# Kernel optimization log

Measured on AMD Instinct MI355X. Metric: run time of the kernel, lower is better.

The kernel has to match this reference:

```python
import jax, jax.numpy as jnp
import numpy as np

EPS = 1e-5
N_HEADS = 8
NEG = -1e32


def _pos_emb(S, D):
    # CosinePositionalEmbedding: sin/cos fully overwrite the random init for even D
    pos = jnp.arange(S, dtype=jnp.float32)[:, None]
    div = jnp.exp(jnp.arange(0, D, 2, dtype=jnp.float32) * (-np.log(10000.0) / D))
    pe = jnp.zeros((S, D), dtype=jnp.float32)
    pe = pe.at[:, 0::2].set(jnp.sin(pos * div))
    pe = pe.at[:, 1::2].set(jnp.cos(pos * div))
    return pe


def _ln(x, g, b):
    mu = jnp.mean(x, axis=-1, keepdims=True)
    var = jnp.mean((x - mu) ** 2, axis=-1, keepdims=True)
    return (x - mu) / jnp.sqrt(var + EPS) * g + b


def setup_inputs() -> dict:
    key = jax.random.key(0)
    B, S, D, FF, L = 32, 512, 512, 2048, 4
    ks = jax.random.split(key, 8)
    w = 0.02
    return {
        "q_embed_data": jax.random.normal(ks[0], (B, S, D), jnp.float32),
        "qa_embed_data": jax.random.normal(ks[1], (B, S, D), jnp.float32),
        "boost_focus": jax.random.uniform(ks[2], (1,), jnp.float32),
        "Wk": w * jax.random.normal(ks[3], (L, D, D), jnp.float32),
        "bk": jnp.zeros((L, D), jnp.float32),
        "Wv": w * jax.random.normal(ks[4], (L, D, D), jnp.float32),
        "bv": jnp.zeros((L, D), jnp.float32),
        "Wo": w * jax.random.normal(ks[5], (L, D, D), jnp.float32),
        "bo": jnp.zeros((L, D), jnp.float32),
        "ln1_g": jnp.ones((L, D), jnp.float32),
        "ln1_b": jnp.zeros((L, D), jnp.float32),
        "W1": w * jax.random.normal(ks[6], (L, D, FF), jnp.float32),
        "b1": jnp.zeros((L, FF), jnp.float32),
        "W2": w * jax.random.normal(ks[7], (L, FF, D), jnp.float32),
        "b2": jnp.zeros((L, D), jnp.float32),
        "ln2_g": jnp.ones((L, D), jnp.float32),
        "ln2_b": jnp.zeros((L, D), jnp.float32),
    }


def reference(q_embed_data, qa_embed_data, boost_focus, Wk, bk, Wv, bv, Wo, bo,
              ln1_g, ln1_b, W1, b1, W2, b2, ln2_g, ln2_b):
    B, S, D = q_embed_data.shape
    L = Wk.shape[0]
    H = N_HEADS
    dk = D // H
    bf = boost_focus[0]
    pe = _pos_emb(S, D)
    x = q_embed_data + pe[None]          # query/key stream
    y = qa_embed_data + pe[None]         # value stream (fixed across blocks)
    # mask=0: triu(k=0)==0 -> only strictly past positions (j < i) allowed
    allowed = jnp.tril(jnp.ones((S, S), bool), k=-1)
    scale = 1.0 / np.sqrt(dk)
    for l in range(L):
        # kq_same=True: q and k both use k_linear on x -> identical projections
        qk = (x @ Wk[l] + bk[l]).reshape(B, S, H, dk).transpose(0, 2, 1, 3)
        v = (y @ Wv[l] + bv[l]).reshape(B, S, H, dk).transpose(0, 2, 1, 3)
        scores = jnp.einsum('bhid,bhjd->bhij', qk, qk) * scale * (1.0 + bf)
        scores = jnp.where(allowed, scores, NEG)
        probs = jax.nn.softmax(scores, axis=-1)
        probs = probs.at[:, :, 0, :].set(0.0)  # zero_pad: first query row zeroed
        attn = jnp.einsum('bhij,bhjd->bhid', probs, v)
        attn = attn.transpose(0, 2, 1, 3).reshape(B, S, D) @ Wo[l] + bo[l]
        x = _ln(x + attn, ln1_g[l], ln1_b[l])
        ff = jax.nn.relu(x @ W1[l] + b1[l]) @ W2[l] + b2[l]
        x = _ln(x + ff, ln2_g[l], ln2_b[l])
    return x
```

## Files before the change

### kernel.cpp

```cpp
#include <hip/hip_runtime.h>
#include <hip/hip_bf16.h>

typedef __bf16 bf16_t;
typedef __bf16 bf16x4 __attribute__((ext_vector_type(4)));
typedef __bf16 bf16x8 __attribute__((ext_vector_type(8)));
typedef float f32x4 __attribute__((ext_vector_type(4)));

union FragU { bf16x8 v; bf16x4 h[2]; };
union F4U { float4 v; float f[4]; };

constexpr int BB = 32, SS = 512, DD = 512, FFD = 2048, LL = 4, HH = 8;

__device__ __forceinline__ int permk(int k) {
  int g = (k >> 2) & 7;
  int pos = (g < 4) ? (g << 1) : (((g - 4) << 1) | 1);
  return (k & ~31) | (pos << 2) | (k & 3);
}

__device__ __forceinline__ void gload_lds16(const bf16_t* g, bf16_t* l) {
  __builtin_amdgcn_global_load_lds(
      (const __attribute__((address_space(1))) void*)g,
      (__attribute__((address_space(3))) void*)l, 16, 0, 0);
}

template<int N> __device__ __forceinline__ void vmwait() {
  asm volatile("s_waitcnt vmcnt(%0)" :: "n"(N) : "memory");
}
__device__ __forceinline__ void lgkmwait0() {
  asm volatile("s_waitcnt lgkmcnt(0)" ::: "memory");
}
__device__ __forceinline__ void barrier_raw() {
  asm volatile("s_barrier" ::: "memory");
}

#define MFMA_ACC(d, a, b) d = __builtin_amdgcn_mfma_f32_16x16x32_bf16((a).v, (b).v, d, 0, 0, 0)

__global__ void pe_kernel(float* __restrict__ pe) {
  int idx = blockIdx.x * blockDim.x + threadIdx.x;
  if (idx >= SS * DD / 2) return;
  int p = idx % (DD / 2);
  int s = idx / (DD / 2);
  float div = expf((float)(2 * p) * (-9.210340371976184f / (float)DD));
  float a = (float)s * div;
  pe[s * DD + 2 * p]     = sinf(a);
  pe[s * DD + 2 * p + 1] = cosf(a);
}

__global__ __launch_bounds__(256) void tcast_kernel(const float* __restrict__ src,
                                                    bf16_t* __restrict__ dst,
                                                    int K, int N) {
  __shared__ float tile[32][33];
  size_t mat = (size_t)blockIdx.z * (size_t)K * (size_t)N;
  int k0 = blockIdx.y * 32, n0 = blockIdx.x * 32;
  int t = threadIdx.x;
  int r = t >> 3, c4 = (t & 7) * 4;
  const float4 v = *reinterpret_cast<const float4*>(&src[mat + (size_t)(k0 + r) * N + n0 + c4]);
  tile[r][c4 + 0] = v.x; tile[r][c4 + 1] = v.y; tile[r][c4 + 2] = v.z; tile[r][c4 + 3] = v.w;
  __syncthreads();
  bf16x4 o;
  o[0] = (bf16_t)tile[c4 + 0][r];
  o[1] = (bf16_t)tile[c4 + 1][r];
  o[2] = (bf16_t)tile[c4 + 2][r];
  o[3] = (bf16_t)tile[c4 + 3][r];
  *reinterpret_cast<bf16x4*>(&dst[mat + permk((n0 + r) * K + k0 + c4)]) = o;
}

__global__ void addpe_kernel(const float* __restrict__ q, const float* __restrict__ qa,
                             const float* __restrict__ pe,
                             float* __restrict__ x, bf16_t* __restrict__ xb,
                             bf16_t* __restrict__ yb) {
  int i = blockIdx.x * blockDim.x + threadIdx.x;
  int pei = i & (SS * DD / 4 - 1);
  float4 pv = reinterpret_cast<const float4*>(pe)[pei];
  float4 qv = reinterpret_cast<const float4*>(q)[i];
  float4 av = reinterpret_cast<const float4*>(qa)[i];
  float4 xv = make_float4(qv.x + pv.x, qv.y + pv.y, qv.z + pv.z, qv.w + pv.w);
  float4 yv = make_float4(av.x + pv.x, av.y + pv.y, av.z + pv.z, av.w + pv.w);
  reinterpret_cast<float4*>(x)[i] = xv;
  bf16x4 xo, yo;
  xo[0] = (bf16_t)xv.x; xo[1] = (bf16_t)xv.y; xo[2] = (bf16_t)xv.z; xo[3] = (bf16_t)xv.w;
  yo[0] = (bf16_t)yv.x; yo[1] = (bf16_t)yv.y; yo[2] = (bf16_t)yv.z; yo[3] = (bf16_t)yv.w;
  int kp = permk(4 * i);
  *reinterpret_cast<bf16x4*>(&xb[kp]) = xo;
  *reinterpret_cast<bf16x4*>(&yb[kp]) = yo;
}

template<int OMODE, bool RELU>
__global__ __launch_bounds__(256, 2) void gemm_kernel(const bf16_t* __restrict__ A,
                                                      const bf16_t* __restrict__ Bt,
                                                      const float* __restrict__ bias,
                                                      void* __restrict__ Cout,
                                                      int N, int K, int nnt) {
  __shared__ bf16_t a_s[2][128 * 64];
  __shared__ bf16_t b_s[2][128 * 64];
  const int t = threadIdx.x;
  const int nwg = gridDim.x;
  const int bid = blockIdx.x;
  const int wg = (bid & 7) * (nwg >> 3) + (bid >> 3);
  const int m0 = (wg / nnt) * 128, n0 = (wg % nnt) * 128;
  const int l = t & 63, w = t >> 6, g = l >> 4, ln = l & 15;
  const int wm = (w >> 1) * 64, wn = (w & 1) * 64;
  const int tr = t >> 3;
  const int bsrc = ((t & 7) ^ (tr & 7)) * 8;
  const bf16_t* Asrc = A + (size_t)(m0 + tr) * K + bsrc;
  const bf16_t* Bsrc = Bt + (size_t)(n0 + tr) * K + bsrc;
  const size_t rstr = (size_t)32 * K;
  const int x0 = (g ^ (ln & 7)) * 8;
  const int x1 = ((4 + g) ^ (ln & 7)) * 8;

  auto STAGE = [&](int p, int T) {
    const int k0 = T << 6;
#pragma unroll
    for (int i = 0; i < 4; i++) gload_lds16(Asrc + k0 + i * rstr, &a_s[p][(i * 256 + t) * 8]);
#pragma unroll
    for (int i = 0; i < 4; i++) gload_lds16(Bsrc + k0 + i * rstr, &b_s[p][(i * 256 + t) * 8]);
  };

  f32x4 acc[4][4] = {};
  const int NT = K >> 6;
  STAGE(0, 0);
  STAGE(1, 1);
  for (int T = 0; T < NT; T++) {
    const int p = T & 1;
    if (T + 1 < NT) vmwait<8>(); else vmwait<0>();
    barrier_raw();
    __builtin_amdgcn_sched_barrier(0);
#pragma unroll
    for (int kc = 0; kc < 2; kc++) {
      const int xo = kc ? x1 : x0;
      FragU fa[4], fb[4];
#pragma unroll
      for (int mi = 0; mi < 4; mi++)
        fa[mi].v = *reinterpret_cast<const bf16x8*>(&a_s[p][(wm + mi * 16 + ln) * 64 + xo]);
#pragma unroll
      for (int ni = 0; ni < 4; ni++)
        fb[ni].v = *reinterpret_cast<const bf16x8*>(&b_s[p][(wn + ni * 16 + ln) * 64 + xo]);
      __builtin_amdgcn_s_setprio(1);
#pragma unroll
      for (int mi = 0; mi < 4; mi++)
#pragma unroll
        for (int ni = 0; ni < 4; ni++)
          MFMA_ACC(acc[mi][ni], fa[mi], fb[ni]);
      __builtin_amdgcn_s_setprio(0);
    }
    __builtin_amdgcn_sched_barrier(0);
    barrier_raw();
    if (T + 2 < NT) STAGE(p, T + 2);
  }

  if constexpr (OMODE == 2) {
    const int brow = m0 >> 9;
    const int s0b = (m0 & 511) + wm;
    bf16_t* vout = reinterpret_cast<bf16_t*>(Cout);
#pragma unroll
    for (int ni = 0; ni < 4; ni++) {
      const int d = n0 + wn + ni * 16 + ln;
      const float bv = bias[d];
      const int h = d >> 6, dd = d & 63;
      bf16_t* vrow = vout + ((size_t)((brow * HH + h) * 64 + dd)) * SS;
#pragma unroll
      for (int mi = 0; mi < 4; mi++) {
        const int s0 = s0b + mi * 16 + g * 4;
        const int jt = s0 >> 6, jj = s0 & 63;
        const int js = jj >> 5, half = (jj >> 4) & 1;
        const int blkx = (js * 4 + g) ^ (dd & 7);
        bf16x4 o;
#pragma unroll
        for (int r = 0; r < 4; r++) o[r] = (bf16_t)(acc[mi][ni][r] + bv);
        *reinterpret_cast<bf16x4*>(&vrow[jt * 64 + blkx * 8 + half * 4]) = o;
      }
    }
  } else {
#pragma unroll
    for (int ni = 0; ni < 4; ni++) {
      const int col = n0 + wn + ni * 16 + ln;
      const float bv = bias[col];
      const int colp = (OMODE == 1) ? permk(col) : col;
#pragma unroll
      for (int mi = 0; mi < 4; mi++)
#pragma unroll
        for (int r = 0; r < 4; r++) {
          int row = m0 + wm + mi * 16 + g * 4 + r;
          float o = acc[mi][ni][r] + bv;
          if (RELU) o = fmaxf(o, 0.f);
          if (OMODE == 1)
            reinterpret_cast<bf16_t*>(Cout)[(size_t)row * N + colp] = (bf16_t)o;
          else
            reinterpret_cast<float*>(Cout)[(size_t)row * N + col] = o;
        }
    }
  }
}

__global__ __launch_bounds__(512, 1) void gemmW_kernel(const bf16_t* __restrict__ A,
                                                       const bf16_t* __restrict__ Bt,
                                                       const float* __restrict__ bias,
                                                       bf16_t* __restrict__ Cout,
                                                       int N, int K, int nnt) {
  __shared__ bf16_t a_s[2][256 * 64];
  __shared__ bf16_t b_s[2][256 * 64];
  const int t = threadIdx.x;
  const int bid = blockIdx.x, nwg = gridDim.x;
  const int wg = (bid & 7) * (nwg >> 3) + (bid >> 3);
  const int m0 = (wg / nnt) * 256, n0 = (wg % nnt) * 256;
  const int l = t & 63, w = t >> 6, g = l >> 4, ln = l & 15, lnx = l & 7;
  const int wr = w >> 2, wc = w & 3;
  const int tr = t >> 3;
  const int bsrc = ((t & 7) ^ (tr & 7)) * 8;
  const bf16_t* Asrc = A + (size_t)(m0 + tr) * K + bsrc;
  const bf16_t* Bsrc = Bt + (size_t)(n0 + tr) * K + bsrc;
  const size_t rstr = (size_t)64 * K;
  const int x0 = (g ^ lnx) * 8;
  const int x1 = ((4 + g) ^ lnx) * 8;

  auto STA = [&](int q, int T2, int i) {
    gload_lds16(Asrc + (T2 << 6) + i * rstr, &a_s[q][(i * 512 + t) * 8]);
  };
  auto STB = [&](int q, int T2, int i) {
    gload_lds16(Bsrc + (T2 << 6) + i * rstr, &b_s[q][(i * 512 + t) * 8]);
  };

  f32x4 acc[8][4] = {};
  const int NT = K >> 6;
#pragma unroll
  for (int i = 0; i < 4; i++) { STA(0, 0, i); STB(0, 0, i); }
#pragma unroll
  for (int i = 0; i < 4; i++) { STA(1, 1, i); STB(1, 1, i); }
  vmwait<8>();
  barrier_raw();

  for (int T = 0; T < NT; T++) {
    const int p = T & 1;
    const bool st = (T + 2) < NT;
    FragU fa[4], fb[4];
#pragma unroll
    for (int mf = 0; mf < 4; mf++)
      fa[mf].v = *reinterpret_cast<const bf16x8*>(&a_s[p][(wr * 128 + mf * 16 + ln) * 64 + x0]);
#pragma unroll
    for (int nf = 0; nf < 4; nf++)
      fb[nf].v = *reinterpret_cast<const bf16x8*>(&b_s[p][(wc * 64 + nf * 16 + ln) * 64 + x0]);
    barrier_raw();
    lgkmwait0();
    __builtin_amdgcn_sched_barrier(0);
    __builtin_amdgcn_s_setprio(1);
#pragma unroll
    for (int mf = 0; mf < 4; mf++)
#pragma unroll
      for (int nf = 0; nf < 4; nf++) MFMA_ACC(acc[mf][nf], fa[mf], fb[nf]);
    __builtin_amdgcn_s_setprio(0);
    barrier_raw();
#pragma unroll
    for (int mf = 0; mf < 4; mf++)
      fa[mf].v = *reinterpret_cast<const bf16x8*>(&a_s[p][(wr * 128 + 64 + mf * 16 + ln) * 64 + x0]);
    barrier_raw();
    lgkmwait0();
    __builtin_amdgcn_sched_barrier(0);
    __builtin_amdgcn_s_setprio(1);
#pragma unroll
    for (int mf = 0; mf < 4; mf++)
#pragma unroll
      for (int nf = 0; nf < 4; nf++) MFMA_ACC(acc[4 + mf][nf], fa[mf], fb[nf]);
    __builtin_amdgcn_s_setprio(0);
    barrier_raw();
#pragma unroll
    for (int mf = 0; mf < 4; mf++)
      fa[mf].v = *reinterpret_cast<const bf16x8*>(&a_s[p][(wr * 128 + mf * 16 + ln) * 64 + x1]);
#pragma unroll
    for (int nf = 0; nf < 4; nf++)
      fb[nf].v = *reinterpret_cast<const bf16x8*>(&b_s[p][(wc * 64 + nf * 16 + ln) * 64 + x1]);
    barrier_raw();
    if (st) { STA(p, T + 2, 0); STA(p, T + 2, 2); STB(p, T + 2, 0); STB(p, T + 2, 1); STB(p, T + 2, 2); STB(p, T + 2, 3); }
    lgkmwait0();
    __builtin_amdgcn_sched_barrier(0);
    __builtin_amdgcn_s_setprio(1);
#pragma unroll
    for (int mf = 0; mf < 4; mf++)
#pragma unroll
      for (int nf = 0; nf < 4; nf++) MFMA_ACC(acc[mf][nf], fa[mf], fb[nf]);
    __builtin_amdgcn_s_setprio(0);
    barrier_raw();
#pragma unroll
    for (int mf = 0; mf < 4; mf++)
      fa[mf].v = *reinterpret_cast<const bf16x8*>(&a_s[p][(wr * 128 + 64 + mf * 16 + ln) * 64 + x1]);
    barrier_raw();
    if (st) { STA(p, T + 2, 1); STA(p, T + 2, 3); }
    lgkmwait0();
    __builtin_amdgcn_sched_barrier(0);
    __builtin_amdgcn_s_setprio(1);
#pragma unroll
    for (int mf = 0; mf < 4; mf++)
#pragma unroll
      for (int nf = 0; nf < 4; nf++) MFMA_ACC(acc[4 + mf][nf], fa[mf], fb[nf]);
    __builtin_amdgcn_s_setprio(0);
    if (T + 1 < NT) { if (st) vmwait<8>(); else vmwait<0>(); }
    barrier_raw();
  }

#pragma unroll
  for (int nf = 0; nf < 4; nf++) {
    const int col = n0 + wc * 64 + nf * 16 + ln;
    const float bv = bias[col];
    const int colp = permk(col);
#pragma unroll
    for (int mf = 0; mf < 8; mf++)
#pragma unroll
      for (int r = 0; r < 4; r++) {
        int row = m0 + wr * 128 + mf * 16 + g * 4 + r;
        float o = fmaxf(acc[mf][nf][r] + bv, 0.f);
        Cout[(size_t)row * N + colp] = (bf16_t)o;
      }
  }
}

__global__ __launch_bounds__(256) void ln_kernel(const float* __restrict__ xin,
                                                 const float* __restrict__ addv,
                                                 const float* __restrict__ gamma,
                                                 const float* __restrict__ beta,
                                                 float* __restrict__ xout,
                                                 bf16_t* __restrict__ xbout) {
  int row = blockIdx.x * 4 + (threadIdx.x >> 6);
  int l = threadIdx.x & 63;
  const float* px = xin + (size_t)row * DD;
  const float* pa = addv + (size_t)row * DD;
  float vals[8];
  float s = 0.f;
#pragma unroll
  for (int i = 0; i < 2; i++) {
    float4 a = reinterpret_cast<const float4*>(px)[l * 2 + i];
    float4 b = reinterpret_cast<const float4*>(pa)[l * 2 + i];
    vals[i * 4 + 0] = a.x + b.x;
    vals[i * 4 + 1] = a.y + b.y;
    vals[i * 4 + 2] = a.z + b.z;
    vals[i * 4 + 3] = a.w + b.w;
  }
#pragma unroll
  for (int j = 0; j < 8; j++) s += vals[j];
#pragma unroll
  for (int off = 1; off < 64; off <<= 1) s += __shfl_xor(s, off, 64);
  float mean = s * (1.f / DD);
  float sq = 0.f;
#pragma unroll
  for (int j = 0; j < 8; j++) { float d = vals[j] - mean; sq += d * d; }
#pragma unroll
  for (int off = 1; off < 64; off <<= 1) sq += __shfl_xor(sq, off, 64);
  float rstd = rsqrtf(sq * (1.f / DD) + 1e-5f);
#pragma unroll
  for (int i = 0; i < 2; i++) {
    F4U o; bf16x4 ob;
#pragma unroll
    for (int j = 0; j < 4; j++) {
      int colj = l * 8 + i * 4 + j;
      float v = (vals[i * 4 + j] - mean) * rstd * gamma[colj] + beta[colj];
      o.f[j] = v;
      ob[j] = (bf16_t)v;
    }
    reinterpret_cast<float4*>(xout + (size_t)row * DD)[l * 2 + i] = o.v;
    *reinterpret_cast<bf16x4*>(&xbout[(size_t)row * DD + permk(l * 8 + i * 4)]) = ob;
  }
}

__global__ __launch_bounds__(256) void attn_kernel(const bf16_t* __restrict__ qk,
                                                   const bf16_t* __restrict__ vtg,
                                                   bf16_t* __restrict__ outp,
                                                   const float* __restrict__ bfp) {
  __shared__ bf16_t k_s[2][64 * 64];
  __shared__ bf16_t v_t[2][64 * 64];
  const int bx = blockIdx.x, h = blockIdx.y, b = blockIdx.z;
  const int t = threadIdx.x, l = t & 63, w = t >> 6, g = l >> 4, ln = l & 15;
  const float sc = 0.125f * (1.f + bfp[0]);
  const size_t base = ((size_t)b * SS) * DD + h * 64;
  const bf16_t* vbase = vtg + ((size_t)((b * HH + h) * 64)) * SS;
  const int NQT = SS / 64;

  auto STAGEKV = [&](int q, int j0) {
    int c1 = t + 256;
    int jr0 = t >> 3, bb0 = t & 7;
    int jr1 = c1 >> 3, bb1 = c1 & 7;
    gload_lds16(qk + base + (size_t)(j0 + jr0) * DD + ((bb0 ^ (jr0 & 7)) * 8), &k_s[q][t * 8]);
    gload_lds16(qk + base + (size_t)(j0 + jr1) * DD + ((bb1 ^ (jr1 & 7)) * 8), &k_s[q][c1 * 8]);
    gload_lds16(vbase + (size_t)jr0 * SS + j0 + bb0 * 8, &v_t[q][t * 8]);
    gload_lds16(vbase + (size_t)jr1 * SS + j0 + bb1 * 8, &v_t[q][c1 * 8]);
  };

  for (int pass = 0; pass < 2; pass++) {
    const int qt = pass ? (NQT - 1 - bx) : bx;
    const int i0 = qt * 64;
    STAGEKV(0, 0);
    FragU qB[2];
    {
      const bf16_t* qp = qk + base + (size_t)(i0 + w * 16 + ln) * DD;
      qB[0].v = *reinterpret_cast<const bf16x8*>(&qp[g * 8]);
      qB[1].v = *reinterpret_cast<const bf16x8*>(&qp[32 + g * 8]);
    }
    float m = -1e30f, lrow = 0.f;
    f32x4 acc[4] = {};
    const int iql = w * 16 + ln;

    for (int kt = 0; kt <= qt; kt++) {
      const int j0 = kt * 64;
      const int p = kt & 1;
      if (kt < qt) { STAGEKV(p ^ 1, j0 + 64); vmwait<4>(); }
      else vmwait<0>();
      barrier_raw();
      __builtin_amdgcn_sched_barrier(0);
      f32x4 sfr[4] = {};
#pragma unroll
      for (int ks = 0; ks < 2; ks++)
#pragma unroll
        for (int nj = 0; nj < 4; nj++) {
          int jc = nj * 16 + ln;
          FragU ka;
          ka.v = *reinterpret_cast<const bf16x8*>(&k_s[p][jc * 64 + (((ks * 4 + g) ^ (jc & 7)) * 8)]);
          sfr[nj] = __builtin_amdgcn_mfma_f32_16x16x32_bf16(ka.v, qB[ks].v, sfr[nj], 0, 0, 0);
        }
      if (kt == qt) {
#pragma unroll
        for (int nj = 0; nj < 4; nj++)
#pragma unroll
          for (int r = 0; r < 4; r++)
            if (nj * 16 + g * 4 + r >= iql) sfr[nj][r] = -1e30f;
      }
      float pm = -1e30f;
#pragma unroll
      for (int nj = 0; nj < 4; nj++)
#pragma unroll
        for (int r = 0; r < 4; r++) pm = fmaxf(pm, sfr[nj][r]);
      pm = fmaxf(pm, __shfl_xor(pm, 16, 64));
      pm = fmaxf(pm, __shfl_xor(pm, 32, 64));
      float mnew = fmaxf(m, pm);
      float fac = __expf(sc * (m - mnew));
      m = mnew;
      float ps = 0.f;
#pragma unroll
      for (int nj = 0; nj < 4; nj++)
#pragma unroll
        for (int r = 0; r < 4; r++) {
          float p2 = __expf(sc * (sfr[nj][r] - m));
          sfr[nj][r] = p2;
          ps += p2;
        }
      ps += __shfl_xor(ps, 16, 64);
      ps += __shfl_xor(ps, 32, 64);
      lrow = lrow * fac + ps;
      float facr[4];
#pragma unroll
      for (int r = 0; r < 4; r++) facr[r] = __shfl(fac, g * 4 + r, 64);
#pragma unroll
      for (int nd = 0; nd < 4; nd++)
#pragma unroll
        for (int r = 0; r < 4; r++) acc[nd][r] *= facr[r];
      FragU pa[2];
#pragma unroll
      for (int js = 0; js < 2; js++)
#pragma unroll
        for (int kk = 0; kk < 4; kk++) {
          pa[js].v[kk]     = (bf16_t)sfr[js * 2][kk];
          pa[js].v[kk + 4] = (bf16_t)sfr[js * 2 + 1][kk];
        }
#pragma unroll
      for (int js = 0; js < 2; js++)
#pragma unroll
        for (int nd = 0; nd < 4; nd++) {
          int d = nd * 16 + ln;
          FragU vb;
          vb.v = *reinterpret_cast<const bf16x8*>(&v_t[p][d * 64 + (((js * 4 + g) ^ (d & 7)) * 8)]);
          acc[nd] = __builtin_amdgcn_mfma_f32_16x16x32_bf16(pa[js].v, vb.v, acc[nd], 0, 0, 0);
        }
      barrier_raw();
    }
    float lr[4];
#pragma unroll
    for (int r = 0; r < 4; r++) lr[r] = __shfl(lrow, g * 4 + r, 64);
    const int orow0 = i0 + w * 16 + g * 4;
#pragma unroll
    for (int nd = 0; nd < 4; nd++) {
      const int colp = permk(nd * 16 + ln);
#pragma unroll
      for (int r = 0; r < 4; r++) {
        int grow = orow0 + r;
        float o = (grow > 0 && lr[r] > 0.f) ? acc[nd][r] / lr[r] : 0.f;
        outp[base + (size_t)grow * DD + colp] = (bf16_t)o;
      }
    }
  }
}

extern "C" void kernel_launch(void* const* d_in, const int* in_sizes, int n_in,
                              void* d_out, int out_size, void* d_ws, size_t ws_size,
                              hipStream_t stream) {
  const float* q_emb  = (const float*)d_in[0];
  const float* qa_emb = (const float*)d_in[1];
  const float* bfp    = (const float*)d_in[2];
  const float* Wk  = (const float*)d_in[3];
  const float* bk  = (const float*)d_in[4];
  const float* Wv  = (const float*)d_in[5];
  const float* bv  = (const float*)d_in[6];
  const float* Wo  = (const float*)d_in[7];
  const float* bo  = (const float*)d_in[8];
  const float* g1  = (const float*)d_in[9];
  const float* be1 = (const float*)d_in[10];
  const float* W1  = (const float*)d_in[11];
  const float* b1  = (const float*)d_in[12];
  const float* W2  = (const float*)d_in[13];
  const float* b2  = (const float*)d_in[14];
  const float* g2  = (const float*)d_in[15];
  const float* be2 = (const float*)d_in[16];
  float* out = (float*)d_out;
  (void)in_sizes; (void)n_in; (void)out_size; (void)ws_size;

  char* wsp = (char*)d_ws;
  size_t off = 0;
  auto alloc = [&](size_t bytes) -> void* {
    void* p = wsp + off;
    off += (bytes + 255) & ~(size_t)255;
    return p;
  };
  const size_t BSD = (size_t)BB * SS * DD;
  float*  pe   = (float*) alloc((size_t)SS * DD * 4);
  float*  x    = (float*) alloc(BSD * 4);
  float*  tmp  = (float*) alloc(BSD * 4);
  bf16_t* xb   = (bf16_t*)alloc(BSD * 2);
  bf16_t* yb   = (bf16_t*)alloc(BSD * 2);
  bf16_t* qkb  = (bf16_t*)alloc(BSD * 2);
  bf16_t* vtg  = (bf16_t*)alloc(BSD * 2);
  bf16_t* atb  = (bf16_t*)alloc(BSD * 2);
  bf16_t* h1   = (bf16_t*)alloc((size_t)BB * SS * FFD * 2);
  bf16_t* Wkb  = (bf16_t*)alloc((size_t)LL * DD * DD * 2);
  bf16_t* Wvb  = (bf16_t*)alloc((size_t)LL * DD * DD * 2);
  bf16_t* Wob  = (bf16_t*)alloc((size_t)LL * DD * DD * 2);
  bf16_t* W1b  = (bf16_t*)alloc((size_t)LL * DD * FFD * 2);
  bf16_t* W2b  = (bf16_t*)alloc((size_t)LL * FFD * DD * 2);

  pe_kernel<<<(SS * DD / 2 + 255) / 256, 256, 0, stream>>>(pe);
  tcast_kernel<<<dim3(DD / 32, DD / 32, LL), 256, 0, stream>>>(Wk, Wkb, DD, DD);
  tcast_kernel<<<dim3(DD / 32, DD / 32, LL), 256, 0, stream>>>(Wv, Wvb, DD, DD);
  tcast_kernel<<<dim3(DD / 32, DD / 32, LL), 256, 0, stream>>>(Wo, Wob, DD, DD);
  tcast_kernel<<<dim3(FFD / 32, DD / 32, LL), 256, 0, stream>>>(W1, W1b, DD, FFD);
  tcast_kernel<<<dim3(DD / 32, FFD / 32, LL), 256, 0, stream>>>(W2, W2b, FFD, DD);
  addpe_kernel<<<(int)(BSD / 4 / 256), 256, 0, stream>>>(q_emb, qa_emb, pe, x, xb, yb);

  const int M = BB * SS;
  const int nD = (M / 128) * (DD / 128);
  const int nW = (M / 256) * (FFD / 256);
  dim3 gA(SS / 128, HH, BB);
  for (int layer = 0; layer < LL; layer++) {
    const bf16_t* Wkl = Wkb + (size_t)layer * DD * DD;
    const bf16_t* Wvl = Wvb + (size_t)layer * DD * DD;
    const bf16_t* Wol = Wob + (size_t)layer * DD * DD;
    const bf16_t* W1l = W1b + (size_t)layer * DD * FFD;
    const bf16_t* W2l = W2b + (size_t)layer * FFD * DD;
    gemm_kernel<1, false><<<nD, 256, 0, stream>>>(xb, Wkl, bk + layer * DD, qkb, DD, DD, DD / 128);
    gemm_kernel<2, false><<<nD, 256, 0, stream>>>(yb, Wvl, bv + layer * DD, vtg, DD, DD, DD / 128);
    attn_kernel<<<gA, 256, 0, stream>>>(qkb, vtg, atb, bfp);
    gemm_kernel<0, false><<<nD, 256, 0, stream>>>(atb, Wol, bo + layer * DD, tmp, DD, DD, DD / 128);
    ln_kernel<<<M / 4, 256, 0, stream>>>(x, tmp, g1 + layer * DD, be1 + layer * DD, x, xb);
    gemmW_kernel<<<nW, 512, 0, stream>>>(xb, W1l, b1 + layer * FFD, h1, FFD, DD, FFD / 256);
    gemm_kernel<0, false><<<nD, 256, 0, stream>>>(h1, W2l, b2 + layer * DD, tmp, DD, FFD, DD / 128);
    float* xo = (layer == LL - 1) ? out : x;
    ln_kernel<<<M / 4, 256, 0, stream>>>(x, tmp, g2 + layer * DD, be2 + layer * DD, xo, xb);
  }
}
```

Measured before the change: 887.3 us.

## Keep residual stream in bf16, tile FFN hidden layout, permute LN params

Drops the fp32 residual copy x and the fp32 tmp buffer. LayerNorm now reads bf16 residual and bf16 GEMM output in the permuted column layout, using gamma/beta that are pre-permuted once to match. The W1 GEMM writes h1 in 256x256 tiles that the W2 GEMM reads through a new tiled A-addressing mode, aiming for contiguous loads. This cuts memory traffic in the LN and GEMM epilogues, but the residual now accumulates in bf16, which can cost accuracy.

```diff
diff --git a/kernel.cpp b/kernel.cpp
--- a/kernel.cpp
+++ b/kernel.cpp
@@ -15,6 +15,11 @@
   int g = (k >> 2) & 7;
   int pos = (g < 4) ? (g << 1) : (((g - 4) << 1) | 1);
   return (k & ~31) | (pos << 2) | (k & 3);
+}
+__device__ __forceinline__ int permpos(int c) {
+  int gq = c >> 2;
+  int pos = (gq < 4) ? (gq << 1) : (((gq - 4) << 1) | 1);
+  return pos * 4 + (c & 3);
 }
 
 __device__ __forceinline__ void gload_lds16(const bf16_t* g, bf16_t* l) {
@@ -44,6 +49,16 @@
   float a = (float)s * div;
   pe[s * DD + 2 * p]     = sinf(a);
   pe[s * DD + 2 * p + 1] = cosf(a);
+}
+
+__global__ void gbperm_kernel(const float* __restrict__ g1, const float* __restrict__ b1,
+                              const float* __restrict__ g2, const float* __restrict__ b2,
+                              float* __restrict__ g1p, float* __restrict__ b1p,
+                              float* __restrict__ g2p, float* __restrict__ b2p) {
+  int idx = blockIdx.x * 256 + threadIdx.x;
+  if (idx >= LL * DD) return;
+  int p = (idx & ~511) | permk(idx & 511);
+  g1p[p] = g1[idx]; b1p[p] = b1[idx]; g2p[p] = g2[idx]; b2p[p] = b2[idx];
 }
 
 __global__ __launch_bounds__(256) void tcast_kernel(const float* __restrict__ src,
@@ -67,25 +82,23 @@
 
 __global__ void addpe_kernel(const float* __restrict__ q, const float* __restrict__ qa,
                              const float* __restrict__ pe,
-                             float* __restrict__ x, bf16_t* __restrict__ xb,
-                             bf16_t* __restrict__ yb) {
+                             bf16_t* __restrict__ xb, bf16_t* __restrict__ yb) {
   int i = blockIdx.x * blockDim.x + threadIdx.x;
   int pei = i & (SS * DD / 4 - 1);
   float4 pv = reinterpret_cast<const float4*>(pe)[pei];
   float4 qv = reinterpret_cast<const float4*>(q)[i];
   float4 av = reinterpret_cast<const float4*>(qa)[i];
-  float4 xv = make_float4(qv.x + pv.x, qv.y + pv.y, qv.z + pv.z, qv.w + pv.w);
-  float4 yv = make_float4(av.x + pv.x, av.y + pv.y, av.z + pv.z, av.w + pv.w);
-  reinterpret_cast<float4*>(x)[i] = xv;
   bf16x4 xo, yo;
-  xo[0] = (bf16_t)xv.x; xo[1] = (bf16_t)xv.y; xo[2] = (bf16_t)xv.z; xo[3] = (bf16_t)xv.w;
-  yo[0] = (bf16_t)yv.x; yo[1] = (bf16_t)yv.y; yo[2] = (bf16_t)yv.z; yo[3] = (bf16_t)yv.w;
+  xo[0] = (bf16_t)(qv.x + pv.x); xo[1] = (bf16_t)(qv.y + pv.y);
+  xo[2] = (bf16_t)(qv.z + pv.z); xo[3] = (bf16_t)(qv.w + pv.w);
+  yo[0] = (bf16_t)(av.x + pv.x); yo[1] = (bf16_t)(av.y + pv.y);
+  yo[2] = (bf16_t)(av.z + pv.z); yo[3] = (bf16_t)(av.w + pv.w);
   int kp = permk(4 * i);
   *reinterpret_cast<bf16x4*>(&xb[kp]) = xo;
   *reinterpret_cast<bf16x4*>(&yb[kp]) = yo;
 }
 
-template<int OMODE, bool RELU>
+template<int OMODE, bool RELU, bool ATILED = false>
 __global__ __launch_bounds__(256, 2) void gemm_kernel(const bf16_t* __restrict__ A,
                                                       const bf16_t* __restrict__ Bt,
                                                       const float* __restrict__ bias,
@@ -102,18 +115,27 @@
   const int wm = (w >> 1) * 64, wn = (w & 1) * 64;
   const int tr = t >> 3;
   const int bsrc = ((t & 7) ^ (tr & 7)) * 8;
-  const bf16_t* Asrc = A + (size_t)(m0 + tr) * K + bsrc;
+  const bf16_t* Asrc;
+  size_t arstr;
+  if constexpr (ATILED) {
+    Asrc = A + (size_t)(m0 >> 8) * ((size_t)K * 256) + (size_t)((m0 & 255) + tr) * 256 + bsrc;
+    arstr = 8192;
+  } else {
+    Asrc = A + (size_t)(m0 + tr) * K + bsrc;
+    arstr = (size_t)32 * K;
+  }
   const bf16_t* Bsrc = Bt + (size_t)(n0 + tr) * K + bsrc;
   const size_t rstr = (size_t)32 * K;
   const int x0 = (g ^ (ln & 7)) * 8;
   const int x1 = ((4 + g) ^ (ln & 7)) * 8;
 
   auto STAGE = [&](int p, int T) {
-    const int k0 = T << 6;
-#pragma unroll
-    for (int i = 0; i < 4; i++) gload_lds16(Asrc + k0 + i * rstr, &a_s[p][(i * 256 + t) * 8]);
-#pragma unroll
-    for (int i = 0; i < 4; i++) gload_lds16(Bsrc + k0 + i * rstr, &b_s[p][(i * 256 + t) * 8]);
+    const int ka = ATILED ? ((T >> 2) * 65536 + (T & 3) * 64) : (T << 6);
+    const int kb = T << 6;
+#pragma unroll
+    for (int i = 0; i < 4; i++) gload_lds16(Asrc + ka + i * arstr, &a_s[p][(i * 256 + t) * 8]);
+#pragma unroll
+    for (int i = 0; i < 4; i++) gload_lds16(Bsrc + kb + i * rstr, &b_s[p][(i * 256 + t) * 8]);
   };
 
   f32x4 acc[4][4] = {};
@@ -175,7 +197,7 @@
     for (int ni = 0; ni < 4; ni++) {
       const int col = n0 + wn + ni * 16 + ln;
       const float bv = bias[col];
-      const int colp = (OMODE == 1) ? permk(col) : col;
+      const int colp = permk(col);
 #pragma unroll
       for (int mi = 0; mi < 4; mi++)
 #pragma unroll
@@ -183,10 +205,7 @@
           int row = m0 + wm + mi * 16 + g * 4 + r;
           float o = acc[mi][ni][r] + bv;
           if (RELU) o = fmaxf(o, 0.f);
-          if (OMODE == 1)
-            reinterpret_cast<bf16_t*>(Cout)[(size_t)row * N + colp] = (bf16_t)o;
-          else
-            reinterpret_cast<float*>(Cout)[(size_t)row * N + col] = o;
+          reinterpret_cast<bf16_t*>(Cout)[(size_t)row * N + colp] = (bf16_t)o;
         }
     }
   }
@@ -296,45 +315,41 @@
     barrier_raw();
   }
 
+  const size_t tbase = (size_t)(m0 >> 8) * ((size_t)N * 256) + (size_t)(n0 >> 8) * 65536;
 #pragma unroll
   for (int nf = 0; nf < 4; nf++) {
-    const int col = n0 + wc * 64 + nf * 16 + ln;
-    const float bv = bias[col];
-    const int colp = permk(col);
-#pragma unroll
-    for (int mf = 0; mf < 8; mf++)
+    const int col_l = wc * 64 + nf * 16 + ln;
+    const float bv = bias[n0 + col_l];
+    const int colp = (col_l & ~31) | permpos(col_l & 31);
+#pragma unroll
+    for (int mf = 0; mf < 8; mf++) {
+      const int mloc = wr * 128 + mf * 16 + g * 4;
 #pragma unroll
       for (int r = 0; r < 4; r++) {
-        int row = m0 + wr * 128 + mf * 16 + g * 4 + r;
         float o = fmaxf(acc[mf][nf][r] + bv, 0.f);
-        Cout[(size_t)row * N + colp] = (bf16_t)o;
+        Cout[tbase + (size_t)(mloc + r) * 256 + colp] = (bf16_t)o;
       }
-  }
-}
-
-__global__ __launch_bounds__(256) void ln_kernel(const float* __restrict__ xin,
-                                                 const float* __restrict__ addv,
-                                                 const float* __restrict__ gamma,
-                                                 const float* __restrict__ beta,
-                                                 float* __restrict__ xout,
-                                                 bf16_t* __restrict__ xbout) {
+    }
+  }
+}
+
+template<bool FINAL>
+__global__ __launch_bounds__(256) void lnp_kernel(const bf16_t* __restrict__ xb,
+                                                  const bf16_t* __restrict__ tb,
+                                                  const float* __restrict__ gp,
+                                                  const float* __restrict__ bp,
+                                                  bf16_t* __restrict__ xbo,
+                                                  float* __restrict__ fout) {
   int row = blockIdx.x * 4 + (threadIdx.x >> 6);
   int l = threadIdx.x & 63;
-  const float* px = xin + (size_t)row * DD;
-  const float* pa = addv + (size_t)row * DD;
+  size_t base = (size_t)row * DD + l * 8;
+  FragU xv, tv;
+  xv.v = *reinterpret_cast<const bf16x8*>(&xb[base]);
+  tv.v = *reinterpret_cast<const bf16x8*>(&tb[base]);
   float vals[8];
   float s = 0.f;
 #pragma unroll
-  for (int i = 0; i < 2; i++) {
-    float4 a = reinterpret_cast<const float4*>(px)[l * 2 + i];
-    float4 b = reinterpret_cast<const float4*>(pa)[l * 2 + i];
-    vals[i * 4 + 0] = a.x + b.x;
-    vals[i * 4 + 1] = a.y + b.y;
-    vals[i * 4 + 2] = a.z + b.z;
-    vals[i * 4 + 3] = a.w + b.w;
-  }
-#pragma unroll
-  for (int j = 0; j < 8; j++) s += vals[j];
+  for (int j = 0; j < 8; j++) { vals[j] = (float)xv.v[j] + (float)tv.v[j]; s += vals[j]; }
 #pragma unroll
   for (int off = 1; off < 64; off <<= 1) s += __shfl_xor(s, off, 64);
   float mean = s * (1.f / DD);
@@ -344,18 +359,29 @@
 #pragma unroll
   for (int off = 1; off < 64; off <<= 1) sq += __shfl_xor(sq, off, 64);
   float rstd = rsqrtf(sq * (1.f / DD) + 1e-5f);
-#pragma unroll
-  for (int i = 0; i < 2; i++) {
-    F4U o; bf16x4 ob;
-#pragma unroll
-    for (int j = 0; j < 4; j++) {
-      int colj = l * 8 + i * 4 + j;
-      float v = (vals[i * 4 + j] - mean) * rstd * gamma[colj] + beta[colj];
-      o.f[j] = v;
-      ob[j] = (bf16_t)v;
-    }
-    reinterpret_cast<float4*>(xout + (size_t)row * DD)[l * 2 + i] = o.v;
-    *reinterpret_cast<bf16x4*>(&xbout[(size_t)row * DD + permk(l * 8 + i * 4)]) = ob;
+  F4U g0, g1q, b0, b1q;
+  g0.v  = *reinterpret_cast<const float4*>(&gp[l * 8]);
+  g1q.v = *reinterpret_cast<const float4*>(&gp[l * 8 + 4]);
+  b0.v  = *reinterpret_cast<const float4*>(&bp[l * 8]);
+  b1q.v = *reinterpret_cast<const float4*>(&bp[l * 8 + 4]);
+  float ov[8];
+#pragma unroll
+  for (int j = 0; j < 4; j++) ov[j]     = (vals[j] - mean) * rstd * g0.f[j] + b0.f[j];
+#pragma unroll
+  for (int j = 0; j < 4; j++) ov[4 + j] = (vals[4 + j] - mean) * rstd * g1q.f[j] + b1q.f[j];
+  if (FINAL) {
+    int c = l >> 2, i = l & 3;
+    F4U o0, o1;
+#pragma unroll
+    for (int j = 0; j < 4; j++) { o0.f[j] = ov[j]; o1.f[j] = ov[4 + j]; }
+    float* fr = fout + (size_t)row * DD + c * 32 + 4 * i;
+    *reinterpret_cast<float4*>(fr) = o0.v;
+    *reinterpret_cast<float4*>(fr + 16) = o1.v;
+  } else {
+    FragU ob;
+#pragma unroll
+    for (int j = 0; j < 8; j++) ob.v[j] = (bf16_t)ov[j];
+    *reinterpret_cast<bf16x8*>(&xbo[base]) = ob.v;
   }
 }
 
@@ -517,14 +543,17 @@
   };
   const size_t BSD = (size_t)BB * SS * DD;
   float*  pe   = (float*) alloc((size_t)SS * DD * 4);
-  float*  x    = (float*) alloc(BSD * 4);
-  float*  tmp  = (float*) alloc(BSD * 4);
   bf16_t* xb   = (bf16_t*)alloc(BSD * 2);
   bf16_t* yb   = (bf16_t*)alloc(BSD * 2);
   bf16_t* qkb  = (bf16_t*)alloc(BSD * 2);
   bf16_t* vtg  = (bf16_t*)alloc(BSD * 2);
   bf16_t* atb  = (bf16_t*)alloc(BSD * 2);
+  bf16_t* tmpb = (bf16_t*)alloc(BSD * 2);
   bf16_t* h1   = (bf16_t*)alloc((size_t)BB * SS * FFD * 2);
+  float*  g1p  = (float*) alloc((size_t)LL * DD * 4);
+  float*  b1p  = (float*) alloc((size_t)LL * DD * 4);
+  float*  g2p  = (float*) alloc((size_t)LL * DD * 4);
+  float*  b2p  = (float*) alloc((size_t)LL * DD * 4);
   bf16_t* Wkb  = (bf16_t*)alloc((size_t)LL * DD * DD * 2);
   bf16_t* Wvb  = (bf16_t*)alloc((size_t)LL * DD * DD * 2);
   bf16_t* Wob  = (bf16_t*)alloc((size_t)LL * DD * DD * 2);
@@ -532,12 +561,13 @@
   bf16_t* W2b  = (bf16_t*)alloc((size_t)LL * FFD * DD * 2);
 
   pe_kernel<<<(SS * DD / 2 + 255) / 256, 256, 0, stream>>>(pe);
+  gbperm_kernel<<<(LL * DD + 255) / 256, 256, 0, stream>>>(g1, be1, g2, be2, g1p, b1p, g2p, b2p);
   tcast_kernel<<<dim3(DD / 32, DD / 32, LL), 256, 0, stream>>>(Wk, Wkb, DD, DD);
   tcast_kernel<<<dim3(DD / 32, DD / 32, LL), 256, 0, stream>>>(Wv, Wvb, DD, DD);
   tcast_kernel<<<dim3(DD / 32, DD / 32, LL), 256, 0, stream>>>(Wo, Wob, DD, DD);
   tcast_kernel<<<dim3(FFD / 32, DD / 32, LL), 256, 0, stream>>>(W1, W1b, DD, FFD);
   tcast_kernel<<<dim3(DD / 32, FFD / 32, LL), 256, 0, stream>>>(W2, W2b, FFD, DD);
-  addpe_kernel<<<(int)(BSD / 4 / 256), 256, 0, stream>>>(q_emb, qa_emb, pe, x, xb, yb);
+  addpe_kernel<<<(int)(BSD / 4 / 256), 256, 0, stream>>>(q_emb, qa_emb, pe, xb, yb);
 
   const int M = BB * SS;
   const int nD = (M / 128) * (DD / 128);
@@ -552,11 +582,13 @@
     gemm_kernel<1, false><<<nD, 256, 0, stream>>>(xb, Wkl, bk + layer * DD, qkb, DD, DD, DD / 128);
     gemm_kernel<2, false><<<nD, 256, 0, stream>>>(yb, Wvl, bv + layer * DD, vtg, DD, DD, DD / 128);
     attn_kernel<<<gA, 256, 0, stream>>>(qkb, vtg, atb, bfp);
-    gemm_kernel<0, false><<<nD, 256, 0, stream>>>(atb, Wol, bo + layer * DD, tmp, DD, DD, DD / 128);
-    ln_kernel<<<M / 4, 256, 0, stream>>>(x, tmp, g1 + layer * DD, be1 + layer * DD, x, xb);
+    gemm_kernel<1, false><<<nD, 256, 0, stream>>>(atb, Wol, bo + layer * DD, tmpb, DD, DD, DD / 128);
+    lnp_kernel<false><<<M / 4, 256, 0, stream>>>(xb, tmpb, g1p + layer * DD, b1p + layer * DD, xb, nullptr);
     gemmW_kernel<<<nW, 512, 0, stream>>>(xb, W1l, b1 + layer * FFD, h1, FFD, DD, FFD / 256);
-    gemm_kernel<0, false><<<nD, 256, 0, stream>>>(h1, W2l, b2 + layer * DD, tmp, DD, FFD, DD / 128);
-    float* xo = (layer == LL - 1) ? out : x;
-    ln_kernel<<<M / 4, 256, 0, stream>>>(x, tmp, g2 + layer * DD, be2 + layer * DD, xo, xb);
-  }
-}
+    gemm_kernel<1, false, true><<<nD, 256, 0, stream>>>(h1, W2l, b2 + layer * DD, tmpb, DD, FFD, DD / 128);
+    if (layer == LL - 1)
+      lnp_kernel<true><<<M / 4, 256, 0, stream>>>(xb, tmpb, g2p + layer * DD, b2p + layer * DD, nullptr, out);
+    else
+      lnp_kernel<false><<<M / 4, 256, 0, stream>>>(xb, tmpb, g2p + layer * DD, b2p + layer * DD, xb, nullptr);
+  }
+}
```

Measured after the change: 814.5 us. 8.2% less time.
